# Kernel optimization log

Hardware: AMD Instinct MI355X
Metric: run time of the kernel (lower is better)

The kernel has to match this reference:

```python
import jax, jax.numpy as jnp
import numpy as np

EPS = 1e-6
D_CONV = 4

def _layernorm(x):
    m = jnp.mean(x, axis=-1, keepdims=True)
    v = jnp.mean((x - m) ** 2, axis=-1, keepdims=True)
    return (x - m) / jnp.sqrt(v + EPS)

def setup_inputs() -> dict:
    key = jax.random.key(0)
    ks = jax.random.split(key, 20)
    B, L, D = 2, 4096, 1024
    Di = D          # expand = 1
    N = 16          # d_state
    R = 64          # dt_rank = ceil(D/16)
    H = 4 * D       # mlp hidden
    s = 0.02
    rn = lambda k, sh: s * jax.random.normal(k, sh, dtype=jnp.float32)
    x = jax.random.normal(ks[0], (B, L, D), dtype=jnp.float32)
    path = jax.random.permutation(ks[1], L).astype(jnp.int32)
    path_rev = jnp.argsort(path).astype(jnp.int32)
    A_log = jnp.log(jnp.tile(jnp.arange(1, N + 1, dtype=jnp.float32)[None, :], (Di, 1)))
    return {
        'x': x, 'path': path, 'path_rev': path_rev,
        'in_proj_w': rn(ks[2], (2 * Di, D)),
        'conv_w': rn(ks[3], (Di, D_CONV)), 'conv_b': rn(ks[4], (Di,)),
        'x_proj_w': rn(ks[5], (R + 2 * N, Di)),
        'dt_proj_w': rn(ks[6], (Di, R)), 'dt_proj_b': rn(ks[7], (Di,)),
        'A_log': A_log, 'D_param': jnp.ones((Di,), dtype=jnp.float32),
        'out_proj_w': rn(ks[8], (D, Di)),
        'fc1_w': rn(ks[9], (H, D)), 'fc1_b': jnp.zeros((H,), dtype=jnp.float32),
        'fc2_w': rn(ks[10], (D, H)), 'fc2_b': jnp.zeros((D,), dtype=jnp.float32),
    }

def _mamba(u, in_proj_w, conv_w, conv_b, x_proj_w, dt_proj_w, dt_proj_b, A_log, D_param, out_proj_w):
    B, L, _ = u.shape
    N = A_log.shape[1]
    R = dt_proj_w.shape[1]
    xz = u @ in_proj_w.T                      # (B,L,2*Di)
    xi, z = jnp.split(xz, 2, axis=-1)
    # causal depthwise conv1d, kernel 4
    xpad = jnp.pad(xi, ((0, 0), (D_CONV - 1, 0), (0, 0)))
    xc = conv_b + sum(conv_w[:, k] * xpad[:, k:k + L, :] for k in range(D_CONV))
    xc = jax.nn.silu(xc)                      # (B,L,Di)
    proj = xc @ x_proj_w.T                    # (B,L,R+2N)
    dt_r = proj[..., :R]
    Bm = proj[..., R:R + N]                   # (B,L,N)
    Cm = proj[..., R + N:]                    # (B,L,N)
    dt = jax.nn.softplus(dt_r @ dt_proj_w.T + dt_proj_b)  # (B,L,Di)
    A = -jnp.exp(A_log)                       # (Di,N)

    def step(h, inp):
        dt_t, B_t, C_t, x_t = inp             # (B,Di),(B,N),(B,N),(B,Di)
        dA = jnp.exp(dt_t[:, :, None] * A)    # (B,Di,N)
        h = dA * h + (dt_t * x_t)[:, :, None] * B_t[:, None, :]
        y = jnp.einsum('bdn,bn->bd', h, C_t)
        return h, y

    h0 = jnp.zeros((B, xc.shape[-1], N), dtype=u.dtype)
    xs = (dt.transpose(1, 0, 2), Bm.transpose(1, 0, 2), Cm.transpose(1, 0, 2), xc.transpose(1, 0, 2))
    _, ys = jax.lax.scan(step, h0, xs)        # (L,B,Di)
    y = ys.transpose(1, 0, 2) + D_param * xc
    y = y * jax.nn.silu(z)
    return y @ out_proj_w.T

def reference(x, path, path_rev, in_proj_w, conv_w, conv_b, x_proj_w, dt_proj_w, dt_proj_b,
              A_log, D_param, out_proj_w, fc1_w, fc1_b, fc2_w, fc2_b):
    tmp1 = x[:, path, :]                      # zigzag gather
    tmp1 = _mamba(_layernorm(tmp1), in_proj_w, conv_w, conv_b, x_proj_w,
                  dt_proj_w, dt_proj_b, A_log, D_param, out_proj_w)
    x = x + tmp1[:, path_rev, :]              # zigzag scatter (inverse gather)
    h = _layernorm(x)
    h = jax.nn.gelu(h @ fc1_w.T + fc1_b, approximate=True) @ fc2_w.T + fc2_b
    return x + h
```

## Files before the change

### kernel.cpp

```cpp
#include <hip/hip_runtime.h>
#include <cstdint>
#include <cstddef>

typedef unsigned short u16;
typedef __bf16 bf16x8 __attribute__((ext_vector_type(8)));
typedef float f32x4 __attribute__((ext_vector_type(4)));

#define B_ 2
#define L_ 4096
#define D_ 1024
#define N_ 16
#define BL_ 8192
#define NC_ 64
#define LC_ 64

__device__ __forceinline__ float bf2f(u16 h) {
  union { unsigned int u; float f; } v; v.u = ((unsigned int)h) << 16; return v.f;
}
__device__ __forceinline__ u16 f2bf(float f) {
  union { float f; unsigned int u; } v; v.f = f;
  unsigned int r = v.u + 0x7FFFu + ((v.u >> 16) & 1u);
  return (u16)(r >> 16);
}
__device__ __forceinline__ float sigmoidf_(float x) { return 1.0f / (1.0f + __expf(-x)); }

#define WBF_TOT 11730944
__global__ __launch_bounds__(256) void cvt_w_k(
    const float* __restrict__ s0, const float* __restrict__ s1,
    const float* __restrict__ s2, const float* __restrict__ s3,
    const float* __restrict__ s4, const float* __restrict__ s5,
    u16* __restrict__ dst)
{
  int i = blockIdx.x * 256 + threadIdx.x;
  if (i >= WBF_TOT) return;
  float v;
  if (i < 2097152) v = s0[i];
  else if (i < 2228224) { int j = i - 2097152; v = (j < 98304) ? s1[j] : 0.0f; }
  else if (i < 2293760) v = s2[i - 2228224];
  else if (i < 3342336) v = s3[i - 2293760];
  else if (i < 7536640) v = s4[i - 3342336];
  else v = s5[i - 7536640];
  dst[i] = f2bf(v);
}

#define BM 128
#define BN 128
#define BK 32

enum { M_BF16 = 0, M_PROJ = 1, M_SOFTPLUS = 2, M_GELU = 3, M_BIASRES = 4 };

#define GLDS(gp, lp) __builtin_amdgcn_global_load_lds( \
    (const __attribute__((address_space(1))) void*)(gp), \
    (__attribute__((address_space(3))) void*)(lp), 16, 0, 0)

template<int MODE, int K>
__global__ __launch_bounds__(256) void gemm_bt(
    const u16* __restrict__ A, const u16* __restrict__ W,
    float* __restrict__ C, u16* __restrict__ C2,
    const float* __restrict__ bias, const u16* __restrict__ resid,
    int M, int N)
{
  __shared__ __align__(16) u16 As[3][BM * BK];
  __shared__ __align__(16) u16 Bs[3][BN * BK];

  const int id = blockIdx.x + gridDim.x * blockIdx.y;
  const int xcd = id & 7;
  const int qq = id >> 3;
  const int bandH = gridDim.y >> 3;
  const int xs = qq % gridDim.x;
  const int ys = xcd * bandH + qq / gridDim.x;
  const int bm = ys * BM;
  const int bn = xs * BN;

  const int tid = threadIdx.x;
  const int lane = tid & 63;
  const int wave = tid >> 6;
  const int wr = (wave >> 1) * 64;
  const int wc = (wave & 1) * 64;

  f32x4 acc[4][4];
#pragma unroll
  for (int i = 0; i < 4; ++i)
#pragma unroll
    for (int j = 0; j < 4; ++j)
#pragma unroll
      for (int r = 0; r < 4; ++r) acc[i][j][r] = 0.0f;

  const int r0 = tid >> 2;
  const int ke = (((tid & 3) ^ (r0 & 3)) << 3);
  const u16* Ab = A + (size_t)(bm + r0) * K + ke;
  const u16* Wb = W + (size_t)(bn + r0) * K + ke;
  constexpr size_t rstep = (size_t)64 * K;

  auto issue = [&](int buf, int k0) {
    GLDS(Ab + k0, &As[buf][tid * 8]);
    GLDS(Ab + k0 + rstep, &As[buf][(tid + 256) * 8]);
    GLDS(Wb + k0, &Bs[buf][tid * 8]);
    GLDS(Wb + k0 + rstep, &Bs[buf][(tid + 256) * 8]);
  };

  issue(0, 0);
  if constexpr (BK < K) issue(1, BK);

  const int mr = lane & 15;
  const int pos = (((lane >> 4) ^ (mr & 3)) << 3);
  constexpr int NIT = K / BK;

  auto step = [&](int it) {
    if (it + 1 < NIT) asm volatile("s_waitcnt vmcnt(4)" ::: "memory");
    else              asm volatile("s_waitcnt vmcnt(0)" ::: "memory");
    asm volatile("s_barrier" ::: "memory");
    if (it + 2 < NIT) issue((it + 2) % 3, (it + 2) * BK);
    const int cur = it % 3;
    bf16x8 af[4], bfr[4];
#pragma unroll
    for (int i = 0; i < 4; ++i)
      af[i] = *(const bf16x8*)(&As[cur][(wr + i * 16 + mr) * BK + pos]);
#pragma unroll
    for (int j = 0; j < 4; ++j)
      bfr[j] = *(const bf16x8*)(&Bs[cur][(wc + j * 16 + mr) * BK + pos]);
#pragma unroll
    for (int i = 0; i < 4; ++i)
#pragma unroll
      for (int j = 0; j < 4; ++j)
        acc[i][j] = __builtin_amdgcn_mfma_f32_16x16x32_bf16(af[i], bfr[j], acc[i][j], 0, 0, 0);
  };

  if constexpr (NIT <= 32) {
#pragma unroll
    for (int it = 0; it < NIT; ++it) step(it);
  } else {
#pragma unroll 6
    for (int it = 0; it < NIT; ++it) step(it);
  }

  const int mlo = (lane >> 4) << 2;
  const int nlo = lane & 15;
#pragma unroll
  for (int i = 0; i < 4; ++i) {
#pragma unroll
    for (int j = 0; j < 4; ++j) {
      int col = bn + wc + j * 16 + nlo;
      if (col < N) {
#pragma unroll
        for (int r = 0; r < 4; ++r) {
          int row = bm + wr + i * 16 + mlo + r;
          float v = acc[i][j][r];
          if constexpr (MODE == M_BF16) {
            C2[(size_t)row * N + col] = f2bf(v);
          } else if constexpr (MODE == M_PROJ) {
            C[(size_t)row * 96 + col] = v;
            if (col < 64) C2[((size_t)row << 6) + col] = f2bf(v);
          } else if constexpr (MODE == M_SOFTPLUS) {
            v += bias[col];
            v = (v > 20.0f) ? v : log1pf(__expf(v));
            C2[(size_t)row * N + col] = f2bf(v);
          } else if constexpr (MODE == M_GELU) {
            v += bias[col];
            float a = 0.7978845608028654f * (v + 0.044715f * v * v * v);
            float t = 1.0f - 2.0f / (__expf(2.0f * a) + 1.0f);
            C2[(size_t)row * N + col] = f2bf(0.5f * v * (1.0f + t));
          } else if constexpr (MODE == M_BIASRES) {
            C[(size_t)row * N + col] = v + bias[col] + bf2f(resid[(size_t)row * N + col]);
          }
        }
      }
    }
  }
}

__device__ __forceinline__ void blockReduce2(float& s, float& q) {
#pragma unroll
  for (int o = 32; o > 0; o >>= 1) { s += __shfl_down(s, o, 64); q += __shfl_down(q, o, 64); }
  __shared__ float red[2][4];
  int lane = threadIdx.x & 63, wave = threadIdx.x >> 6;
  if (lane == 0) { red[0][wave] = s; red[1][wave] = q; }
  __syncthreads();
  s = red[0][0] + red[0][1] + red[0][2] + red[0][3];
  q = red[1][0] + red[1][1] + red[1][2] + red[1][3];
}

__global__ __launch_bounds__(256) void ln_gather_k(
    const float* __restrict__ x, const int* __restrict__ path, u16* __restrict__ out)
{
  int b = blockIdx.x >> 12;
  int l = blockIdx.x & 4095;
  int src = path[l];
  const float* row = x + (((size_t)b * L_ + src) << 10);
  u16* orow = out + (((size_t)b * L_ + l) << 10);
  float v[4], s = 0.f, q = 0.f;
#pragma unroll
  for (int i = 0; i < 4; ++i) {
    v[i] = row[threadIdx.x + (i << 8)];
    s += v[i]; q += v[i] * v[i];
  }
  blockReduce2(s, q);
  float mean = s * (1.0f / 1024.0f);
  float var = q * (1.0f / 1024.0f) - mean * mean;
  float rstd = rsqrtf(var + 1e-6f);
#pragma unroll
  for (int i = 0; i < 4; ++i)
    orow[threadIdx.x + (i << 8)] = f2bf((v[i] - mean) * rstd);
}

__global__ __launch_bounds__(256) void ln_scatter_k(
    const float* __restrict__ x, const int* __restrict__ prev,
    const u16* __restrict__ mo, u16* __restrict__ xnew, u16* __restrict__ lnout)
{
  int b = blockIdx.x >> 12;
  int l = blockIdx.x & 4095;
  int pl = prev[l];
  const float* xr = x + (((size_t)b * L_ + l) << 10);
  const u16* mr_ = mo + (((size_t)b * L_ + pl) << 10);
  size_t base = ((size_t)blockIdx.x) << 10;
  float v[4], s = 0.f, q = 0.f;
#pragma unroll
  for (int i = 0; i < 4; ++i) {
    v[i] = xr[threadIdx.x + (i << 8)] + bf2f(mr_[threadIdx.x + (i << 8)]);
    s += v[i]; q += v[i] * v[i];
  }
  blockReduce2(s, q);
  float mean = s * (1.0f / 1024.0f);
  float var = q * (1.0f / 1024.0f) - mean * mean;
  float rstd = rsqrtf(var + 1e-6f);
#pragma unroll
  for (int i = 0; i < 4; ++i) {
    xnew[base + threadIdx.x + (i << 8)] = f2bf(v[i]);
    lnout[base + threadIdx.x + (i << 8)] = f2bf((v[i] - mean) * rstd);
  }
}

__global__ __launch_bounds__(256) void conv_silu_k(
    const u16* __restrict__ xz, const float* __restrict__ cw, const float* __restrict__ cb,
    u16* __restrict__ xc)
{
  int idx = blockIdx.x * 256 + threadIdx.x;
  int d = idx & 1023;
  int l = (idx >> 10) & 4095;
  int b = idx >> 22;
  float acc = cb[d];
#pragma unroll
  for (int k = 0; k < 4; ++k) {
    int ls = l + k - 3;
    if (ls >= 0)
      acc += cw[(d << 2) + k] * bf2f(xz[(((size_t)b * L_ + ls) << 11) + d]);
  }
  acc = acc * sigmoidf_(acc);
  xc[idx] = f2bf(acc);
}

__global__ __launch_bounds__(256) void scan_p1_k(
    const u16* __restrict__ dt, const u16* __restrict__ xc, const float* __restrict__ proj,
    const float* __restrict__ A_log, float* __restrict__ acum, float* __restrict__ hloc)
{
  int c = blockIdx.x & (NC_ - 1);
  int q = (blockIdx.x >> 6) & 3;
  int b = blockIdx.x >> 8;
  int d = (q << 8) + threadIdx.x;
  float Arow[N_];
#pragma unroll
  for (int n = 0; n < N_; ++n) Arow[n] = -__expf(A_log[(d << 4) + n]);
  float h[N_], ac[N_];
#pragma unroll
  for (int n = 0; n < N_; ++n) { h[n] = 0.0f; ac[n] = 1.0f; }
  int l0 = c << 6;
  for (int i = 0; i < LC_; ++i) {
    size_t rowb = (size_t)b * L_ + (l0 + i);
    float dtv = bf2f(dt[(rowb << 10) + d]);
    float xv = bf2f(xc[(rowb << 10) + d]);
    float dtx = dtv * xv;
    const float* Bp = proj + rowb * 96 + 64;
#pragma unroll
    for (int n = 0; n < N_; ++n) {
      float dA = __expf(dtv * Arow[n]);
      h[n] = dA * h[n] + dtx * Bp[n];
      ac[n] *= dA;
    }
  }
  size_t sb = ((((size_t)b << 10) + d) << 10) + (c << 4);
#pragma unroll
  for (int n = 0; n < N_; ++n) { acum[sb + n] = ac[n]; hloc[sb + n] = h[n]; }
}

__global__ __launch_bounds__(256) void scan_p2_k(
    const float* __restrict__ acum, const float* __restrict__ hloc, float* __restrict__ hin)
{
  int idx = blockIdx.x * 256 + threadIdx.x;
  int n = idx & 15;
  int dn = idx >> 4;
  size_t base = ((size_t)dn << 10) + n;
  float hs = 0.0f;
  for (int c = 0; c < NC_; ++c) {
    hin[base + (c << 4)] = hs;
    hs = acum[base + (c << 4)] * hs + hloc[base + (c << 4)];
  }
}

__global__ __launch_bounds__(256) void scan_p3_k(
    const u16* __restrict__ dt, const u16* __restrict__ xc, const float* __restrict__ proj,
    const float* __restrict__ A_log, const float* __restrict__ Dp, const float* __restrict__ hin,
    const u16* __restrict__ xz, u16* __restrict__ yg)
{
  int c = blockIdx.x & (NC_ - 1);
  int q = (blockIdx.x >> 6) & 3;
  int b = blockIdx.x >> 8;
  int d = (q << 8) + threadIdx.x;
  float Arow[N_];
#pragma unroll
  for (int n = 0; n < N_; ++n) Arow[n] = -__expf(A_log[(d << 4) + n]);
  float h[N_];
  size_t sb = ((((size_t)b << 10) + d) << 10) + (c << 4);
#pragma unroll
  for (int n = 0; n < N_; ++n) h[n] = hin[sb + n];
  float Dv = Dp[d];
  int l0 = c << 6;
  for (int i = 0; i < LC_; ++i) {
    size_t rowb = (size_t)b * L_ + (l0 + i);
    float dtv = bf2f(dt[(rowb << 10) + d]);
    float xv = bf2f(xc[(rowb << 10) + d]);
    float dtx = dtv * xv;
    const float* Bp = proj + rowb * 96 + 64;
    const float* Cp = proj + rowb * 96 + 80;
    float y = 0.0f;
#pragma unroll
    for (int n = 0; n < N_; ++n) {
      float dA = __expf(dtv * Arow[n]);
      h[n] = dA * h[n] + dtx * Bp[n];
      y += h[n] * Cp[n];
    }
    y += Dv * xv;
    float zv = bf2f(xz[(rowb << 11) + 1024 + d]);
    yg[(rowb << 10) + d] = f2bf(y * zv * sigmoidf_(zv));
  }
}

extern "C" void kernel_launch(void* const* d_in, const int* in_sizes, int n_in,
                              void* d_out, int out_size, void* d_ws, size_t ws_size,
                              hipStream_t stream)
{
  const float* x_in      = (const float*)d_in[0];
  const int*   path      = (const int*)d_in[1];
  const int*   path_rev  = (const int*)d_in[2];
  const float* in_proj_w = (const float*)d_in[3];
  const float* conv_w    = (const float*)d_in[4];
  const float* conv_b    = (const float*)d_in[5];
  const float* x_proj_w  = (const float*)d_in[6];
  const float* dt_proj_w = (const float*)d_in[7];
  const float* dt_proj_b = (const float*)d_in[8];
  const float* A_log     = (const float*)d_in[9];
  const float* Dp        = (const float*)d_in[10];
  const float* out_pw    = (const float*)d_in[11];
  const float* fc1_w     = (const float*)d_in[12];
  const float* fc1_b     = (const float*)d_in[13];
  const float* fc2_w     = (const float*)d_in[14];
  const float* fc2_b     = (const float*)d_in[15];
  float* out = (float*)d_out;

  char* w = (char*)d_ws;
  size_t off = 0;
  auto alloc = [&](size_t bytes) -> char* {
    char* p = w + off;
    off = (off + bytes + 255) & ~(size_t)255;
    return p;
  };
  u16*   wbf   = (u16*)  alloc((size_t)WBF_TOT * 2);
  u16*   ln_bf = (u16*)  alloc((size_t)BL_ * 1024 * 2);
  u16*   xz    = (u16*)  alloc((size_t)BL_ * 2048 * 2);
  u16*   xc    = (u16*)  alloc((size_t)BL_ * 1024 * 2);
  char*  pool0 = alloc(0);
  float* proj  = (float*)alloc((size_t)BL_ * 96 * 4);
  u16*   dtr   = (u16*)  alloc((size_t)BL_ * 64 * 2);
  u16*   dt    = (u16*)  alloc((size_t)BL_ * 1024 * 2);
  float* acum  = (float*)alloc((size_t)2 * 1024 * NC_ * 16 * 4);
  float* hloc  = (float*)alloc((size_t)2 * 1024 * NC_ * 16 * 4);
  float* hin   = (float*)alloc((size_t)2 * 1024 * NC_ * 16 * 4);
  u16*   yg    = (u16*)  alloc((size_t)BL_ * 1024 * 2);
  u16*   h1b   = (u16*)pool0;
  off = (size_t)(pool0 - w) + ((size_t)BL_ * 4096 * 2);
  u16*   xnew  = (u16*)  alloc((size_t)BL_ * 1024 * 2);
  u16*   mo    = xz;

  const u16* w_inp = wbf;
  const u16* w_xp  = wbf + 2097152;
  const u16* w_dtp = wbf + 2228224;
  const u16* w_op  = wbf + 2293760;
  const u16* w_fc1 = wbf + 3342336;
  const u16* w_fc2 = wbf + 7536640;

  dim3 blk(256);
  cvt_w_k<<<WBF_TOT / 256, blk, 0, stream>>>(in_proj_w, x_proj_w, dt_proj_w, out_pw,
                                             fc1_w, fc2_w, wbf);
  ln_gather_k<<<BL_, blk, 0, stream>>>(x_in, path, ln_bf);
  gemm_bt<M_BF16, 1024><<<dim3(16, 64), blk, 0, stream>>>(ln_bf, w_inp, nullptr, xz, nullptr, nullptr, 8192, 2048);
  conv_silu_k<<<(BL_ * 1024) / 256, blk, 0, stream>>>(xz, conv_w, conv_b, xc);
  gemm_bt<M_PROJ, 1024><<<dim3(1, 64), blk, 0, stream>>>(xc, w_xp, proj, dtr, nullptr, nullptr, 8192, 96);
  gemm_bt<M_SOFTPLUS, 64><<<dim3(8, 64), blk, 0, stream>>>(dtr, w_dtp, nullptr, dt, dt_proj_b, nullptr, 8192, 1024);
  scan_p1_k<<<2 * 4 * NC_, blk, 0, stream>>>(dt, xc, proj, A_log, acum, hloc);
  scan_p2_k<<<(2 * 1024 * 16) / 256, blk, 0, stream>>>(acum, hloc, hin);
  scan_p3_k<<<2 * 4 * NC_, blk, 0, stream>>>(dt, xc, proj, A_log, Dp, hin, xz, yg);
  gemm_bt<M_BF16, 1024><<<dim3(8, 64), blk, 0, stream>>>(yg, w_op, nullptr, mo, nullptr, nullptr, 8192, 1024);
  ln_scatter_k<<<BL_, blk, 0, stream>>>(x_in, path_rev, mo, xnew, ln_bf);
  gemm_bt<M_GELU, 1024><<<dim3(32, 64), blk, 0, stream>>>(ln_bf, w_fc1, nullptr, h1b, fc1_b, nullptr, 8192, 4096);
  gemm_bt<M_BIASRES, 4096><<<dim3(8, 64), blk, 0, stream>>>(h1b, w_fc2, out, nullptr, fc2_b, xnew, 8192, 1024);
}
```

Baseline: 624.2 us.

## Add 128x256-tile GEMM kernel for the large projections and MLP

Introduces a gemm_big kernel with 128x256 output tiles, each wave computing a 64x128 sub-tile with 4x8 MFMA fragments, and uses it for in_proj, out_proj, fc1 and fc2. The epilogue is factored into a shared helper. The larger tiles raise arithmetic intensity per LDS load and cut global reloads of A. In exchange, register pressure rises and grids shrink, so the narrower GEMMs launch only 256 blocks and may underfill the GPU.

```diff
diff --git a/kernel.cpp b/kernel.cpp
--- a/kernel.cpp
+++ b/kernel.cpp
@@ -43,15 +43,40 @@
   dst[i] = f2bf(v);
 }
 
-#define BM 128
-#define BN 128
 #define BK 32
-
 enum { M_BF16 = 0, M_PROJ = 1, M_SOFTPLUS = 2, M_GELU = 3, M_BIASRES = 4 };
 
 #define GLDS(gp, lp) __builtin_amdgcn_global_load_lds( \
     (const __attribute__((address_space(1))) void*)(gp), \
     (__attribute__((address_space(3))) void*)(lp), 16, 0, 0)
+
+template<int MODE>
+__device__ __forceinline__ void epi_store(
+    float v, size_t row, int col, int Nn,
+    float* __restrict__ C, u16* __restrict__ C2,
+    const float* __restrict__ bias, const u16* __restrict__ resid)
+{
+  if constexpr (MODE == M_BF16) {
+    C2[row * Nn + col] = f2bf(v);
+  } else if constexpr (MODE == M_PROJ) {
+    C[row * 96 + col] = v;
+    if (col < 64) C2[(row << 6) + col] = f2bf(v);
+  } else if constexpr (MODE == M_SOFTPLUS) {
+    v += bias[col];
+    v = (v > 20.0f) ? v : log1pf(__expf(v));
+    C2[row * Nn + col] = f2bf(v);
+  } else if constexpr (MODE == M_GELU) {
+    v += bias[col];
+    float a = 0.7978845608028654f * (v + 0.044715f * v * v * v);
+    float t = 1.0f - 2.0f / (__expf(2.0f * a) + 1.0f);
+    C2[row * Nn + col] = f2bf(0.5f * v * (1.0f + t));
+  } else if constexpr (MODE == M_BIASRES) {
+    C[row * Nn + col] = v + bias[col] + bf2f(resid[row * Nn + col]);
+  }
+}
+
+#define BM 128
+#define BN 128
 
 template<int MODE, int K>
 __global__ __launch_bounds__(256) void gemm_bt(
@@ -144,26 +169,111 @@
       if (col < N) {
 #pragma unroll
         for (int r = 0; r < 4; ++r) {
-          int row = bm + wr + i * 16 + mlo + r;
-          float v = acc[i][j][r];
-          if constexpr (MODE == M_BF16) {
-            C2[(size_t)row * N + col] = f2bf(v);
-          } else if constexpr (MODE == M_PROJ) {
-            C[(size_t)row * 96 + col] = v;
-            if (col < 64) C2[((size_t)row << 6) + col] = f2bf(v);
-          } else if constexpr (MODE == M_SOFTPLUS) {
-            v += bias[col];
-            v = (v > 20.0f) ? v : log1pf(__expf(v));
-            C2[(size_t)row * N + col] = f2bf(v);
-          } else if constexpr (MODE == M_GELU) {
-            v += bias[col];
-            float a = 0.7978845608028654f * (v + 0.044715f * v * v * v);
-            float t = 1.0f - 2.0f / (__expf(2.0f * a) + 1.0f);
-            C2[(size_t)row * N + col] = f2bf(0.5f * v * (1.0f + t));
-          } else if constexpr (MODE == M_BIASRES) {
-            C[(size_t)row * N + col] = v + bias[col] + bf2f(resid[(size_t)row * N + col]);
-          }
+          size_t row = (size_t)(bm + wr + i * 16 + mlo + r);
+          epi_store<MODE>(acc[i][j][r], row, col, N, C, C2, bias, resid);
         }
+      }
+    }
+  }
+}
+
+#define BM2 128
+#define BN2 256
+
+template<int MODE, int K>
+__global__ __launch_bounds__(256, 2) void gemm_big(
+    const u16* __restrict__ A, const u16* __restrict__ W,
+    float* __restrict__ C, u16* __restrict__ C2,
+    const float* __restrict__ bias, const u16* __restrict__ resid,
+    int M, int N)
+{
+  __shared__ __align__(16) u16 As[3][BM2 * BK];
+  __shared__ __align__(16) u16 Bs[3][BN2 * BK];
+
+  const int id = blockIdx.x + gridDim.x * blockIdx.y;
+  const int xcd = id & 7;
+  const int qq = id >> 3;
+  const int bandH = gridDim.y >> 3;
+  const int xs = qq % gridDim.x;
+  const int ys = xcd * bandH + qq / gridDim.x;
+  const int bm = ys * BM2;
+  const int bn = xs * BN2;
+
+  const int tid = threadIdx.x;
+  const int lane = tid & 63;
+  const int wave = tid >> 6;
+  const int wm = (wave >> 1) * 64;
+  const int wn = (wave & 1) * 128;
+
+  f32x4 acc[4][8];
+#pragma unroll
+  for (int i = 0; i < 4; ++i)
+#pragma unroll
+    for (int j = 0; j < 8; ++j)
+#pragma unroll
+      for (int r = 0; r < 4; ++r) acc[i][j][r] = 0.0f;
+
+  const int r0 = tid >> 2;
+  const int ke = (((tid & 3) ^ (r0 & 3)) << 3);
+  const u16* Ab = A + (size_t)(bm + r0) * K + ke;
+  const u16* Wb = W + (size_t)(bn + r0) * K + ke;
+  constexpr size_t rstep = (size_t)64 * K;
+
+  auto issue = [&](int buf, int k0) {
+    GLDS(Ab + k0, &As[buf][tid * 8]);
+    GLDS(Ab + k0 + rstep, &As[buf][(tid + 256) * 8]);
+    GLDS(Wb + k0, &Bs[buf][tid * 8]);
+    GLDS(Wb + k0 + rstep,     &Bs[buf][(tid + 256) * 8]);
+    GLDS(Wb + k0 + 2 * rstep, &Bs[buf][(tid + 512) * 8]);
+    GLDS(Wb + k0 + 3 * rstep, &Bs[buf][(tid + 768) * 8]);
+  };
+
+  issue(0, 0);
+  issue(1, BK);
+
+  const int mr = lane & 15;
+  const int pos = (((lane >> 4) ^ (mr & 3)) << 3);
+  constexpr int NIT = K / BK;
+
+  auto step = [&](int it) {
+    if (it + 1 < NIT) asm volatile("s_waitcnt vmcnt(6)" ::: "memory");
+    else              asm volatile("s_waitcnt vmcnt(0)" ::: "memory");
+    asm volatile("s_barrier" ::: "memory");
+    if (it + 2 < NIT) issue((it + 2) % 3, (it + 2) * BK);
+    const int cur = it % 3;
+    bf16x8 af[4], bfr[8];
+#pragma unroll
+    for (int i = 0; i < 4; ++i)
+      af[i] = *(const bf16x8*)(&As[cur][(wm + i * 16 + mr) * BK + pos]);
+#pragma unroll
+    for (int j = 0; j < 8; ++j)
+      bfr[j] = *(const bf16x8*)(&Bs[cur][(wn + j * 16 + mr) * BK + pos]);
+#pragma unroll
+    for (int i = 0; i < 4; ++i)
+#pragma unroll
+      for (int j = 0; j < 8; ++j)
+        acc[i][j] = __builtin_amdgcn_mfma_f32_16x16x32_bf16(af[i], bfr[j], acc[i][j], 0, 0, 0);
+  };
+
+  if constexpr (NIT <= 32) {
+#pragma unroll
+    for (int it = 0; it < NIT; ++it) step(it);
+  } else {
+#pragma unroll 6
+    for (int it = 0; it < NIT; ++it) step(it);
+  }
+
+  const int mlo = (lane >> 4) << 2;
+  const int nlo = lane & 15;
+#pragma unroll
+  for (int i = 0; i < 4; ++i) {
+#pragma unroll
+    for (int j = 0; j < 8; ++j) {
+      int col = bn + wn + j * 16 + nlo;
+#pragma unroll
+      for (int r = 0; r < 4; ++r) {
+        size_t row = (size_t)(bm + wm + i * 16 + mlo + r);
+        epi_store<MODE>(acc[i][j][r], row, col, N, C, C2, bias, resid);
       }
     }
   }
@@ -391,15 +501,15 @@
   cvt_w_k<<<WBF_TOT / 256, blk, 0, stream>>>(in_proj_w, x_proj_w, dt_proj_w, out_pw,
                                              fc1_w, fc2_w, wbf);
   ln_gather_k<<<BL_, blk, 0, stream>>>(x_in, path, ln_bf);
-  gemm_bt<M_BF16, 1024><<<dim3(16, 64), blk, 0, stream>>>(ln_bf, w_inp, nullptr, xz, nullptr, nullptr, 8192, 2048);
+  gemm_big<M_BF16, 1024><<<dim3(8, 64), blk, 0, stream>>>(ln_bf, w_inp, nullptr, xz, nullptr, nullptr, 8192, 2048);
   conv_silu_k<<<(BL_ * 1024) / 256, blk, 0, stream>>>(xz, conv_w, conv_b, xc);
   gemm_bt<M_PROJ, 1024><<<dim3(1, 64), blk, 0, stream>>>(xc, w_xp, proj, dtr, nullptr, nullptr, 8192, 96);
   gemm_bt<M_SOFTPLUS, 64><<<dim3(8, 64), blk, 0, stream>>>(dtr, w_dtp, nullptr, dt, dt_proj_b, nullptr, 8192, 1024);
   scan_p1_k<<<2 * 4 * NC_, blk, 0, stream>>>(dt, xc, proj, A_log, acum, hloc);
   scan_p2_k<<<(2 * 1024 * 16) / 256, blk, 0, stream>>>(acum, hloc, hin);
   scan_p3_k<<<2 * 4 * NC_, blk, 0, stream>>>(dt, xc, proj, A_log, Dp, hin, xz, yg);
-  gemm_bt<M_BF16, 1024><<<dim3(8, 64), blk, 0, stream>>>(yg, w_op, nullptr, mo, nullptr, nullptr, 8192, 1024);
+  gemm_big<M_BF16, 1024><<<dim3(4, 64), blk, 0, stream>>>(yg, w_op, nullptr, mo, nullptr, nullptr, 8192, 1024);
   ln_scatter_k<<<BL_, blk, 0, stream>>>(x_in, path_rev, mo, xnew, ln_bf);
-  gemm_bt<M_GELU, 1024><<<dim3(32, 64), blk, 0, stream>>>(ln_bf, w_fc1, nullptr, h1b, fc1_b, nullptr, 8192, 4096);
-  gemm_bt<M_BIASRES, 4096><<<dim3(8, 64), blk, 0, stream>>>(h1b, w_fc2, out, nullptr, fc2_b, xnew, 8192, 1024);
-}
+  gemm_big<M_GELU, 1024><<<dim3(16, 64), blk, 0, stream>>>(ln_bf, w_fc1, nullptr, h1b, fc1_b, nullptr, 8192, 4096);
+  gemm_big<M_BIASRES, 4096><<<dim3(4, 64), blk, 0, stream>>>(h1b, w_fc2, out, nullptr, fc2_b, xnew, 8192, 1024);
+}
```

Result: no change. 614.0 us (-1.6%).
